# Kernel optimization log

Hardware: AMD Instinct MI355X
Metric: run time of the kernel (lower is better)

Reference implementation:

```python
import jax, jax.numpy as jnp
import numpy as np

EMB = 1024
FF = 4096
NE = 8
TOPK = 2
TEMP = 1.0


def setup_inputs() -> dict:
    key = jax.random.key(0)
    ks = jax.random.split(key, 8)
    s_emb = 1.0 / np.sqrt(EMB)
    s_ff = 1.0 / np.sqrt(FF)
    x = jax.random.normal(ks[0], (4, 2048, EMB), dtype=jnp.float32)
    gate_W = jax.random.uniform(ks[1], (EMB, NE), minval=-s_emb, maxval=s_emb, dtype=jnp.float32)
    gate_b = jax.random.uniform(ks[2], (NE,), minval=-s_emb, maxval=s_emb, dtype=jnp.float32)
    W1 = jax.random.uniform(ks[3], (NE, EMB, FF), minval=-s_emb, maxval=s_emb, dtype=jnp.float32)
    b1 = jax.random.uniform(ks[4], (NE, FF), minval=-s_emb, maxval=s_emb, dtype=jnp.float32)
    W2 = jax.random.uniform(ks[5], (NE, FF, EMB), minval=-s_ff, maxval=s_ff, dtype=jnp.float32)
    b2 = jax.random.uniform(ks[6], (NE, EMB), minval=-s_ff, maxval=s_ff, dtype=jnp.float32)
    return {"x": x, "gate_W": gate_W, "gate_b": gate_b, "W1": W1, "b1": b1, "W2": W2, "b2": b2}


def reference(x, gate_W, gate_b, W1, b1, W2, b2):
    B, S, D = x.shape
    xf = x.reshape(-1, D)  # [T, D]
    T = xf.shape[0]

    gate_logits = (xf @ gate_W + gate_b) / TEMP            # [T, E]
    gate_scores = jax.nn.softmax(gate_logits, axis=-1)     # [T, E]
    topk_scores, topk_idx = jax.lax.top_k(gate_scores, TOPK)
    topk_scores = topk_scores / jnp.sum(topk_scores, axis=-1, keepdims=True)

    # combine_weights[t, e] = sum_i topk_scores[t, i] * (topk_idx[t, i] == e)
    onehot = jax.nn.one_hot(topk_idx, NE, dtype=xf.dtype)  # [T, K, E]
    combine = jnp.einsum('tk,tke->te', topk_scores, onehot)  # [T, E]

    # Dense per-expert FFN (dropout is identity in eval): h = gelu(x W1 + b1); y = h W2 + b2
    h = jax.nn.gelu(jnp.einsum('td,edf->etf', xf, W1) + b1[:, None, :], approximate=False)
    y = jnp.einsum('etf,efd->etd', h, W2) + b2[:, None, :]  # [E, T, D]
    out = jnp.einsum('te,etd->td', combine, y).reshape(B, S, D)

    # Load-balance auxiliary loss
    expert_counts = jnp.sum(onehot, axis=(0, 1))            # [E]
    expert_fraction = expert_counts / (T * TOPK)
    routing_weights = jnp.mean(gate_scores, axis=0)
    aux_loss = NE * jnp.sum(expert_fraction * routing_weights)
    return out, aux_loss
```

## Files before the change

### kernel.cpp

```cpp
#include <hip/hip_runtime.h>
#include <math.h>

#define EMB 1024
#define FF  4096
#define NE  8
#define TTOK 8192

typedef __attribute__((ext_vector_type(4))) float  f32x4;
typedef __attribute__((ext_vector_type(8))) __bf16 bf16x8;
typedef __attribute__((ext_vector_type(4))) __bf16 bf16x4;

#define MAXROWS  18432

#define WS_COUNTS  0
#define WS_CURSORS 1024
#define WS_SSUM    1056
#define WS_NTILES  2080
#define WS_BASE    2084
#define WS_TILE_E  2176
#define WS_TILE_RB 2816
#define WS_TKIDX   4096
#define WS_TKW     69632
#define WS_SLOT    135168
#define WS_TOKID   200704
#define WS_ROWW    274432
#define WS_BIG2    350208

#define SZ_W1T ((size_t)NE * EMB * FF * 2)
#define SZ_W2T ((size_t)NE * EMB * FF * 2)
#define SZ_XB  ((size_t)TTOK * EMB * 2)
#define SZ_H   ((size_t)MAXROWS * FF * 2)
#define SZ_Y   ((size_t)MAXROWS * EMB * 4)

__device__ inline f32x4 fzero() { f32x4 v = {0.f, 0.f, 0.f, 0.f}; return v; }

__device__ __forceinline__ void gl16(const void* g, void* l) {
    __builtin_amdgcn_global_load_lds(
        (const __attribute__((address_space(1))) void*)g,
        (__attribute__((address_space(3))) void*)l, 16, 0, 0);
}

#define DSR(dst, addr, off) \
    asm volatile("ds_read_b128 %0, %1 offset:" #off : "=v"(dst) : "v"(addr))

__device__ __forceinline__ float gelu_f(float v) {
    float u = fabsf(v) * 0.70710678118654752f;
    float p = 1.0f + u * (0.278393f + u * (0.230389f + u * (0.000972f + u * 0.078108f)));
    p = p * p; p = p * p;
    float er = 1.0f - 1.0f / p;
    float s = (v >= 0.0f) ? er : -er;
    return 0.5f * v * (1.0f + s);
}

__global__ __launch_bounds__(256) void gate_kernel(
    const float* __restrict__ x, const float* __restrict__ gW, const float* __restrict__ gb,
    int* counts, float* ssum, int* tk_idx, float* tk_w, __bf16* __restrict__ xb)
{
    int wave = threadIdx.x >> 6;
    int lane = threadIdx.x & 63;
    int t = blockIdx.x * 4 + wave;

    float acc[NE];
#pragma unroll
    for (int e = 0; e < NE; e++) acc[e] = 0.f;

    const float* xr = x + (size_t)t * EMB;
    __bf16* xbr = xb + (size_t)t * EMB;
#pragma unroll
    for (int i = 0; i < 4; i++) {
        int d0 = i * 256 + lane * 4;
        f32x4 xv = *(const f32x4*)(xr + d0);
        bf16x4 cv;
#pragma unroll
        for (int q = 0; q < 4; q++) cv[q] = (__bf16)xv[q];
        *(bf16x4*)(xbr + d0) = cv;
#pragma unroll
        for (int j = 0; j < 4; j++) {
            const float* wrow = gW + (size_t)(d0 + j) * NE;
            float xs = xv[j];
#pragma unroll
            for (int e = 0; e < NE; e++) acc[e] += xs * wrow[e];
        }
    }
#pragma unroll
    for (int e = 0; e < NE; e++) {
#pragma unroll
        for (int off = 32; off; off >>= 1) acc[e] += __shfl_xor(acc[e], off, 64);
    }
    if (lane == 0) {
        float sc[NE];
        float m = -1e30f;
        for (int e = 0; e < NE; e++) { sc[e] = acc[e] + gb[e]; m = fmaxf(m, sc[e]); }
        float sum = 0.f;
        for (int e = 0; e < NE; e++) { sc[e] = expf(sc[e] - m); sum += sc[e]; }
        float inv = 1.f / sum;
        for (int e = 0; e < NE; e++) sc[e] *= inv;
        int i0 = 0; float s0 = sc[0];
        for (int e = 1; e < NE; e++) if (sc[e] > s0) { s0 = sc[e]; i0 = e; }
        int i1 = -1; float s1 = -1e30f;
        for (int e = 0; e < NE; e++) if (e != i0 && sc[e] > s1) { s1 = sc[e]; i1 = e; }
        float rn = 1.f / (s0 + s1);
        tk_idx[2 * t]     = i0;  tk_idx[2 * t + 1] = i1;
        tk_w[2 * t]       = s0 * rn;  tk_w[2 * t + 1] = s1 * rn;
        int slot = blockIdx.x & 31;
        atomicAdd(&counts[i0 * 32 + slot], 1);
        atomicAdd(&counts[i1 * 32 + slot], 1);
        for (int e = 0; e < NE; e++) atomicAdd(&ssum[e * 32 + slot], sc[e]);
    }
}

__global__ void route_build_kernel(const int* counts, const float* ssum,
                                   int* ntiles, int* base, int* tile_e, int* tile_rb,
                                   float* out_aux)
{
    if (threadIdx.x != 0 || blockIdx.x != 0) return;
    int total = 0, tiles = 0;
    float aux = 0.f;
    for (int e = 0; e < NE; e++) {
        int c = 0; float ss = 0.f;
        for (int j = 0; j < 32; j++) { c += counts[e * 32 + j]; ss += ssum[e * 32 + j]; }
        base[e] = total;
        int nt = (c + 255) >> 8;
        for (int i = 0; i < nt; i++) { tile_e[tiles] = e; tile_rb[tiles] = total + (i << 8); tiles++; }
        total += nt << 8;
        aux += ((float)c / (float)(TTOK * 2)) * (ss / (float)TTOK);
    }
    *ntiles = tiles;
    *out_aux = aux * (float)NE;
}

__global__ __launch_bounds__(256) void scatter_kernel(
    const int* __restrict__ tk_idx, const float* __restrict__ tk_w,
    const int* __restrict__ base, int* cursors, int* token_id, float* roww,
    int* slot_of)
{
    int t = blockIdx.x * 256 + threadIdx.x;
#pragma unroll
    for (int k = 0; k < 2; k++) {
        int e = tk_idx[2 * t + k];
        int pos = atomicAdd(&cursors[e], 1);
        int slot = base[e] + pos;
        token_id[slot] = t;
        roww[slot] = tk_w[2 * t + k];
        slot_of[2 * t + k] = slot;
    }
}

__global__ __launch_bounds__(256) void combine_kernel(
    const float* __restrict__ y0, const float* __restrict__ y1, int nsplit,
    const int* __restrict__ slot_of,
    const int* __restrict__ tk_idx, const float* __restrict__ tk_w,
    const float* __restrict__ b2, float* __restrict__ out)
{
    int t = blockIdx.x;
    int dq = threadIdx.x * 4;
    int s0 = slot_of[2 * t], s1 = slot_of[2 * t + 1];
    int e0 = tk_idx[2 * t], e1 = tk_idx[2 * t + 1];
    float w0 = tk_w[2 * t], w1 = tk_w[2 * t + 1];
    f32x4 ya = *(const f32x4*)(y0 + (size_t)s0 * EMB + dq);
    f32x4 yb = *(const f32x4*)(y0 + (size_t)s1 * EMB + dq);
    if (nsplit == 2) {
        f32x4 za = *(const f32x4*)(y1 + (size_t)s0 * EMB + dq);
        f32x4 zb = *(const f32x4*)(y1 + (size_t)s1 * EMB + dq);
#pragma unroll
        for (int q = 0; q < 4; q++) { ya[q] += za[q]; yb[q] += zb[q]; }
    }
    f32x4 ba = *(const f32x4*)(b2 + (size_t)e0 * EMB + dq);
    f32x4 bb = *(const f32x4*)(b2 + (size_t)e1 * EMB + dq);
    f32x4 r;
#pragma unroll
    for (int q = 0; q < 4; q++) r[q] = w0 * (ya[q] + ba[q]) + w1 * (yb[q] + bb[q]);
    *(f32x4*)(out + (size_t)t * EMB + dq) = r;
}

__global__ __launch_bounds__(256) void transpose_cvt2_kernel(
    const float* __restrict__ W1, __bf16* __restrict__ W1T,
    const float* __restrict__ W2, __bf16* __restrict__ W2T)
{
    int f = blockIdx.x;
    int which = f >> 13; f &= 8191;
    int e = f >> 10; f &= 1023;
    int R, C, bx, by;
    const float* src; __bf16* dst;
    if (which == 0) { R = EMB; C = FF;  bx = f & 15; by = f >> 4; src = W1; dst = W1T; }
    else            { R = FF;  C = EMB; bx = f & 63; by = f >> 6; src = W2; dst = W2T; }
    src += (size_t)e * R * C;
    dst += (size_t)e * R * C;
    __shared__ __bf16 Ls[64 * 72];
    int t = threadIdx.x;
    int r0 = bx * 64, c0 = by * 64;
    int ri = t >> 4, cj = (t & 15) * 4;
#pragma unroll
    for (int p = 0; p < 4; p++) {
        int r = ri + p * 16;
        f32x4 v = *(const f32x4*)(src + (size_t)(r0 + r) * C + c0 + cj);
#pragma unroll
        for (int q = 0; q < 4; q++) Ls[(cj + q) * 72 + r] = (__bf16)v[q];
    }
    __syncthreads();
    int c = t >> 2, rq = (t & 3) * 16;
    bf16x8 a = *(bf16x8*)&Ls[c * 72 + rq];
    bf16x8 b = *(bf16x8*)&Ls[c * 72 + rq + 8];
    *(bf16x8*)(dst + (size_t)(c0 + c) * R + r0 + rq) = a;
    *(bf16x8*)(dst + (size_t)(c0 + c) * R + r0 + rq + 8) = b;
}


__global__ __launch_bounds__(512, 2) void gemm1_8p(
    const __bf16* __restrict__ xb, const __bf16* __restrict__ W1T,
    const float* __restrict__ b1,
    const int* __restrict__ token_id, const int* __restrict__ tile_e,
    const int* __restrict__ tile_rb, const int* __restrict__ ntiles,
    __bf16* __restrict__ h)
{
    extern __shared__ __bf16 lds[];
    int flat = blockIdx.x;
    int c8 = flat & 7, r = flat >> 3;
    int mti = r >> 4, nb = r & 15;
    int mt = c8 * 9 + mti;
    if (mt >= *ntiles) return;
    int e = tile_e[mt], rb = tile_rb[mt];
    int n0 = nb * 256;

    int tid = threadIdx.x, lane = tid & 63, wid = tid >> 6;
    int wr = wid >> 2, wc = wid & 3;
    int cl = lane & 15, cq = lane >> 4;

    int srow = tid >> 2;
    int schunk = (tid & 3) ^ ((tid >> 3) & 3);
    const __bf16* ag[2];
#pragma unroll
    for (int hm = 0; hm < 2; hm++) {
        int tok = token_id[rb + hm * 128 + srow];
        if (tok < 0) tok = 0;
        ag[hm] = xb + (size_t)tok * EMB + schunk * 8;
    }
    const __bf16* bg[2];
#pragma unroll
    for (int hn = 0; hn < 2; hn++)
        bg[hn] = W1T + ((size_t)e * FF + (size_t)(n0 + hn * 128 + srow)) * EMB + schunk * 8;

    int sdA0 = wid * 512, sdA1 = 4096 + wid * 512;
    int sdB0 = 8192 + wid * 512, sdB1 = 12288 + wid * 512;

    uint32_t lb = (uint32_t)(uintptr_t)(__attribute__((address_space(3))) __bf16*)lds;
    int xoffe = (cq ^ ((cl >> 1) & 3)) * 8;
    uint32_t ab0 = lb + 2u * (uint32_t)(wr * 4096 + cl * 32 + xoffe);
    uint32_t bb0 = lb + 2u * (uint32_t)(8192 + (wc >> 1) * 4096 + ((wc & 1) * 64 + cl) * 32 + xoffe);

    f32x4 acc[8][4];
#pragma unroll
    for (int i = 0; i < 8; i++)
#pragma unroll
        for (int j = 0; j < 4; j++) acc[i][j] = fzero();

    const int NT = EMB / 32;
#pragma unroll
    for (int t0 = 0; t0 < 3; t0++) {
        __bf16* bp = lds + t0 * 16384;
        int k0 = t0 * 32;
        gl16(ag[0] + k0, bp + sdA0);
        gl16(ag[1] + k0, bp + sdA1);
        gl16(bg[0] + k0, bp + sdB0);
        gl16(bg[1] + k0, bp + sdB1);
    }
    asm volatile("s_waitcnt vmcnt(8)" ::: "memory");
    __builtin_amdgcn_s_barrier();

#pragma unroll 1
    for (int t = 0; t < NT; t++) {
        uint32_t cboff = (uint32_t)(t & 3) * 32768u;
        uint32_t aaddr = ab0 + cboff, baddr = bb0 + cboff;
        bf16x8 b[4], a[8];
        DSR(b[0], baddr, 0);    DSR(b[1], baddr, 1024);
        DSR(b[2], baddr, 2048); DSR(b[3], baddr, 3072);
        DSR(a[0], aaddr, 0);    DSR(a[1], aaddr, 1024);
        DSR(a[2], aaddr, 2048); DSR(a[3], aaddr, 3072);
        DSR(a[4], aaddr, 4096); DSR(a[5], aaddr, 5120);
        DSR(a[6], aaddr, 6144); DSR(a[7], aaddr, 7168);

        int kt = t + 3;
        if (kt < NT) {
            __bf16* sp = lds + (kt & 3) * 16384;
            int ko = kt * 32;
            gl16(ag[0] + ko, sp + sdA0);
            gl16(ag[1] + ko, sp + sdA1);
            gl16(bg[0] + ko, sp + sdB0);
            gl16(bg[1] + ko, sp + sdB1);
        }

        asm volatile("s_waitcnt lgkmcnt(0)" ::: "memory");
        __builtin_amdgcn_sched_barrier(0);
        __builtin_amdgcn_s_setprio(1);
#pragma unroll
        for (int mi = 0; mi < 8; mi++)
#pragma unroll
            for (int ni = 0; ni < 4; ni++)
                acc[mi][ni] = __builtin_amdgcn_mfma_f32_16x16x32_bf16(a[mi], b[ni], acc[mi][ni], 0, 0, 0);
        __builtin_amdgcn_s_setprio(0);

        if (t < NT - 3)       { asm volatile("s_waitcnt vmcnt(8)" ::: "memory"); }
        else if (t == NT - 3) { asm volatile("s_waitcnt vmcnt(4)" ::: "memory"); }
        else if (t == NT - 2) { asm volatile("s_waitcnt vmcnt(0)" ::: "memory"); }
        if (t < NT - 1) __builtin_amdgcn_s_barrier();
    }

    const float* b1g = b1 + (size_t)e * FF + n0;
#pragma unroll
    for (int mi = 0; mi < 8; mi++) {
#pragma unroll
        for (int ni = 0; ni < 4; ni++) {
            int col = wc * 64 + ni * 16 + cl;
            float bias = b1g[col];
#pragma unroll
            for (int j = 0; j < 4; j++) {
                int row = wr * 128 + mi * 16 + cq * 4 + j;
                float v = acc[mi][ni][j] + bias;
                h[(size_t)(rb + row) * FF + n0 + col] = (__bf16)gelu_f(v);
            }
        }
    }
}

__global__ __launch_bounds__(512, 2) void gemm2_8p(
    const __bf16* __restrict__ h, const __bf16* __restrict__ W2T,
    const int* __restrict__ tile_e, const int* __restrict__ tile_rb,
    const int* __restrict__ ntiles,
    float* __restrict__ y0, float* __restrict__ y1, int nsplit)
{
    extern __shared__ __bf16 lds[];
    int flat = blockIdx.x;
    int c8 = flat & 7, r = flat >> 3;
    int z = r / 36; int r36 = r - z * 36;
    int mti = r36 >> 2, nb = r36 & 3;
    int mt = c8 * 9 + mti;
    if (mt >= *ntiles) return;
    int e = tile_e[mt], rb = tile_rb[mt];
    int n0 = nb * 256;
    int KC = FF / nsplit;
    int koff = z * KC;
    float* y = z ? y1 : y0;

    int tid = threadIdx.x, lane = tid & 63, wid = tid >> 6;
    int wr = wid >> 2, wc = wid & 3;
    int cl = lane & 15, cq = lane >> 4;

    int srow = tid >> 2;
    int schunk = (tid & 3) ^ ((tid >> 3) & 3);
    const __bf16* ag[2];
#pragma unroll
    for (int hm = 0; hm < 2; hm++)
        ag[hm] = h + (size_t)(rb + hm * 128 + srow) * FF + koff + schunk * 8;
    const __bf16* bg[2];
#pragma unroll
    for (int hn = 0; hn < 2; hn++)
        bg[hn] = W2T + ((size_t)e * EMB + (size_t)(n0 + hn * 128 + srow)) * FF + koff + schunk * 8;

    int sdA0 = wid * 512, sdA1 = 4096 + wid * 512;
    int sdB0 = 8192 + wid * 512, sdB1 = 12288 + wid * 512;

    uint32_t lb = (uint32_t)(uintptr_t)(__attribute__((address_space(3))) __bf16*)lds;
    int xoffe = (cq ^ ((cl >> 1) & 3)) * 8;
    uint32_t ab0 = lb + 2u * (uint32_t)(wr * 4096 + cl * 32 + xoffe);
    uint32_t bb0 = lb + 2u * (uint32_t)(8192 + (wc >> 1) * 4096 + ((wc & 1) * 64 + cl) * 32 + xoffe);

    f32x4 acc[8][4];
#pragma unroll
    for (int i = 0; i < 8; i++)
#pragma unroll
        for (int j = 0; j < 4; j++) acc[i][j] = fzero();

    const int NT = KC / 32;
#pragma unroll
    for (int t0 = 0; t0 < 3; t0++) {
        __bf16* bp = lds + t0 * 16384;
        int k0 = t0 * 32;
        gl16(ag[0] + k0, bp + sdA0);
        gl16(ag[1] + k0, bp + sdA1);
        gl16(bg[0] + k0, bp + sdB0);
        gl16(bg[1] + k0, bp + sdB1);
    }
    asm volatile("s_waitcnt vmcnt(8)" ::: "memory");
    __builtin_amdgcn_s_barrier();

#pragma unroll 1
    for (int t = 0; t < NT; t++) {
        uint32_t cboff = (uint32_t)(t & 3) * 32768u;
        uint32_t aaddr = ab0 + cboff, baddr = bb0 + cboff;
        bf16x8 b[4], a[8];
        DSR(b[0], baddr, 0);    DSR(b[1], baddr, 1024);
        DSR(b[2], baddr, 2048); DSR(b[3], baddr, 3072);
        DSR(a[0], aaddr, 0);    DSR(a[1], aaddr, 1024);
        DSR(a[2], aaddr, 2048); DSR(a[3], aaddr, 3072);
        DSR(a[4], aaddr, 4096); DSR(a[5], aaddr, 5120);
        DSR(a[6], aaddr, 6144); DSR(a[7], aaddr, 7168);

        int kt = t + 3;
        if (kt < NT) {
            __bf16* sp = lds + (kt & 3) * 16384;
            int ko = kt * 32;
            gl16(ag[0] + ko, sp + sdA0);
            gl16(ag[1] + ko, sp + sdA1);
            gl16(bg[0] + ko, sp + sdB0);
            gl16(bg[1] + ko, sp + sdB1);
        }

        asm volatile("s_waitcnt lgkmcnt(0)" ::: "memory");
        __builtin_amdgcn_sched_barrier(0);
        __builtin_amdgcn_s_setprio(1);
#pragma unroll
        for (int mi = 0; mi < 8; mi++)
#pragma unroll
            for (int ni = 0; ni < 4; ni++)
                acc[mi][ni] = __builtin_amdgcn_mfma_f32_16x16x32_bf16(a[mi], b[ni], acc[mi][ni], 0, 0, 0);
        __builtin_amdgcn_s_setprio(0);

        if (t < NT - 3)       { asm volatile("s_waitcnt vmcnt(8)" ::: "memory"); }
        else if (t == NT - 3) { asm volatile("s_waitcnt vmcnt(4)" ::: "memory"); }
        else if (t == NT - 2) { asm volatile("s_waitcnt vmcnt(0)" ::: "memory"); }
        if (t < NT - 1) __builtin_amdgcn_s_barrier();
    }

#pragma unroll
    for (int mi = 0; mi < 8; mi++) {
#pragma unroll
        for (int ni = 0; ni < 4; ni++) {
            int col = wc * 64 + ni * 16 + cl;
#pragma unroll
            for (int j = 0; j < 4; j++) {
                int row = wr * 128 + mi * 16 + cq * 4 + j;
                y[(size_t)(rb + row) * EMB + n0 + col] = acc[mi][ni][j];
            }
        }
    }
}

extern "C" void kernel_launch(void* const* d_in, const int* in_sizes, int n_in,
                              void* d_out, int out_size, void* d_ws, size_t ws_size,
                              hipStream_t stream)
{
    const float* x   = (const float*)d_in[0];
    const float* gW  = (const float*)d_in[1];
    const float* gb  = (const float*)d_in[2];
    const float* W1  = (const float*)d_in[3];
    const float* b1  = (const float*)d_in[4];
    const float* W2  = (const float*)d_in[5];
    const float* b2  = (const float*)d_in[6];
    float* out = (float*)d_out;

    char* ws = (char*)d_ws;
    int*   counts  = (int*)(ws + WS_COUNTS);
    int*   cursors = (int*)(ws + WS_CURSORS);
    float* ssum    = (float*)(ws + WS_SSUM);
    int*   ntiles  = (int*)(ws + WS_NTILES);
    int*   base    = (int*)(ws + WS_BASE);
    int*   tile_e  = (int*)(ws + WS_TILE_E);
    int*   tile_rb = (int*)(ws + WS_TILE_RB);
    int*   tk_idx  = (int*)(ws + WS_TKIDX);
    float* tk_w    = (float*)(ws + WS_TKW);
    int*   slot_of = (int*)(ws + WS_SLOT);
    int*   token_id= (int*)(ws + WS_TOKID);
    float* roww    = (float*)(ws + WS_ROWW);

    __bf16* W1T  = (__bf16*)(ws + WS_BIG2);
    __bf16* xb   = (__bf16*)(ws + WS_BIG2 + SZ_W1T);
    __bf16* W2T  = (__bf16*)(ws + WS_BIG2 + SZ_W1T + SZ_XB);
    __bf16* hbuf = (__bf16*)(ws + WS_BIG2 + SZ_W1T + SZ_XB + SZ_W2T);
    size_t fixedend = WS_BIG2 + SZ_W1T + SZ_XB + SZ_W2T;

    float* y0 = (float*)(ws + WS_BIG2);
    float* y1 = (float*)(ws + fixedend + SZ_H);
    int nsplit = (ws_size >= fixedend + SZ_H + SZ_Y) ? 2 : 1;

    hipFuncSetAttribute((const void*)gemm1_8p, hipFuncAttributeMaxDynamicSharedMemorySize, 131072);
    hipFuncSetAttribute((const void*)gemm2_8p, hipFuncAttributeMaxDynamicSharedMemorySize, 131072);

    hipMemsetAsync(ws + WS_COUNTS, 0, 2080, stream);
    hipMemsetAsync(ws + WS_TOKID, 0xFF, (size_t)MAXROWS * 4, stream);

    transpose_cvt2_kernel<<<16384, 256, 0, stream>>>(W1, W1T, W2, W2T);

    gate_kernel<<<TTOK / 4, 256, 0, stream>>>(x, gW, gb, counts, ssum, tk_idx, tk_w, xb);
    route_build_kernel<<<1, 64, 0, stream>>>(counts, ssum, ntiles, base, tile_e, tile_rb,
                                             out + (size_t)TTOK * EMB);
    scatter_kernel<<<TTOK / 256, 256, 0, stream>>>(tk_idx, tk_w, base, cursors, token_id, roww, slot_of);

    gemm1_8p<<<8 * 9 * 16, 512, 131072, stream>>>(
        xb, W1T, b1, token_id, tile_e, tile_rb, ntiles, hbuf);
    gemm2_8p<<<8 * 9 * 4 * nsplit, 512, 131072, stream>>>(
        hbuf, W2T, tile_e, tile_rb, ntiles, y0, y1, nsplit);
    combine_kernel<<<TTOK, 256, 0, stream>>>(y0, y1, nsplit, slot_of, tk_idx, tk_w, b2, out);
}
```

Before: 691.4 us.

## Pre-pack routed token rows for gemm1 and store expert outputs in bf16

Adds a pack kernel that gathers routed token rows of x into a contiguous per-slot buffer, so gemm1 reads its A operand with plain strided addressing instead of gathering through token_id. gemm2 partial outputs are now stored in bf16 rather than fp32, which halves the write and combine read traffic and frees workspace for the packed buffer. The cost is an extra kernel launch plus one more pass over the routed activations, and the bf16 rounding of the split-K partial sums before they are combined.

```diff
diff --git a/kernel.cpp b/kernel.cpp
--- a/kernel.cpp
+++ b/kernel.cpp
@@ -30,7 +30,8 @@
 #define SZ_W2T ((size_t)NE * EMB * FF * 2)
 #define SZ_XB  ((size_t)TTOK * EMB * 2)
 #define SZ_H   ((size_t)MAXROWS * FF * 2)
-#define SZ_Y   ((size_t)MAXROWS * EMB * 4)
+#define SZ_XG  ((size_t)MAXROWS * EMB * 2)
+#define SZ_Y2  ((size_t)MAXROWS * EMB * 2)
 
 __device__ inline f32x4 fzero() { f32x4 v = {0.f, 0.f, 0.f, 0.f}; return v; }
 
@@ -146,8 +147,21 @@
     }
 }
 
+__global__ __launch_bounds__(256) void pack_x_kernel(
+    const __bf16* __restrict__ xb, const int* __restrict__ token_id,
+    __bf16* __restrict__ xg)
+{
+    int tid = threadIdx.x;
+    int slot = blockIdx.x * 2 + (tid >> 7);
+    int off = (tid & 127) * 8;
+    int tok = token_id[slot];
+    uint4 v = {0u, 0u, 0u, 0u};
+    if (tok >= 0) v = *(const uint4*)(xb + (size_t)tok * EMB + off);
+    *(uint4*)(xg + (size_t)slot * EMB + off) = v;
+}
+
 __global__ __launch_bounds__(256) void combine_kernel(
-    const float* __restrict__ y0, const float* __restrict__ y1, int nsplit,
+    const __bf16* __restrict__ y0, const __bf16* __restrict__ y1, int nsplit,
     const int* __restrict__ slot_of,
     const int* __restrict__ tk_idx, const float* __restrict__ tk_w,
     const float* __restrict__ b2, float* __restrict__ out)
@@ -157,13 +171,16 @@
     int s0 = slot_of[2 * t], s1 = slot_of[2 * t + 1];
     int e0 = tk_idx[2 * t], e1 = tk_idx[2 * t + 1];
     float w0 = tk_w[2 * t], w1 = tk_w[2 * t + 1];
-    f32x4 ya = *(const f32x4*)(y0 + (size_t)s0 * EMB + dq);
-    f32x4 yb = *(const f32x4*)(y0 + (size_t)s1 * EMB + dq);
+    bf16x4 va = *(const bf16x4*)(y0 + (size_t)s0 * EMB + dq);
+    bf16x4 vb = *(const bf16x4*)(y0 + (size_t)s1 * EMB + dq);
+    f32x4 ya, yb;
+#pragma unroll
+    for (int q = 0; q < 4; q++) { ya[q] = (float)va[q]; yb[q] = (float)vb[q]; }
     if (nsplit == 2) {
-        f32x4 za = *(const f32x4*)(y1 + (size_t)s0 * EMB + dq);
-        f32x4 zb = *(const f32x4*)(y1 + (size_t)s1 * EMB + dq);
-#pragma unroll
-        for (int q = 0; q < 4; q++) { ya[q] += za[q]; yb[q] += zb[q]; }
+        bf16x4 za = *(const bf16x4*)(y1 + (size_t)s0 * EMB + dq);
+        bf16x4 zb = *(const bf16x4*)(y1 + (size_t)s1 * EMB + dq);
+#pragma unroll
+        for (int q = 0; q < 4; q++) { ya[q] += (float)za[q]; yb[q] += (float)zb[q]; }
     }
     f32x4 ba = *(const f32x4*)(b2 + (size_t)e0 * EMB + dq);
     f32x4 bb = *(const f32x4*)(b2 + (size_t)e1 * EMB + dq);
@@ -206,8 +223,9 @@
 }
 
 
+template <bool PACKED>
 __global__ __launch_bounds__(512, 2) void gemm1_8p(
-    const __bf16* __restrict__ xb, const __bf16* __restrict__ W1T,
+    const __bf16* __restrict__ xsrc, const __bf16* __restrict__ W1T,
     const float* __restrict__ b1,
     const int* __restrict__ token_id, const int* __restrict__ tile_e,
     const int* __restrict__ tile_rb, const int* __restrict__ ntiles,
@@ -231,9 +249,13 @@
     const __bf16* ag[2];
 #pragma unroll
     for (int hm = 0; hm < 2; hm++) {
-        int tok = token_id[rb + hm * 128 + srow];
-        if (tok < 0) tok = 0;
-        ag[hm] = xb + (size_t)tok * EMB + schunk * 8;
+        if (PACKED) {
+            ag[hm] = xsrc + (size_t)(rb + hm * 128 + srow) * EMB + schunk * 8;
+        } else {
+            int tok = token_id[rb + hm * 128 + srow];
+            if (tok < 0) tok = 0;
+            ag[hm] = xsrc + (size_t)tok * EMB + schunk * 8;
+        }
     }
     const __bf16* bg[2];
 #pragma unroll
@@ -326,7 +348,7 @@
     const __bf16* __restrict__ h, const __bf16* __restrict__ W2T,
     const int* __restrict__ tile_e, const int* __restrict__ tile_rb,
     const int* __restrict__ ntiles,
-    float* __restrict__ y0, float* __restrict__ y1, int nsplit)
+    __bf16* __restrict__ y0, __bf16* __restrict__ y1, int nsplit)
 {
     extern __shared__ __bf16 lds[];
     int flat = blockIdx.x;
@@ -339,7 +361,7 @@
     int n0 = nb * 256;
     int KC = FF / nsplit;
     int koff = z * KC;
-    float* y = z ? y1 : y0;
+    __bf16* y = z ? y1 : y0;
 
     int tid = threadIdx.x, lane = tid & 63, wid = tid >> 6;
     int wr = wid >> 2, wc = wid & 3;
@@ -429,7 +451,7 @@
 #pragma unroll
             for (int j = 0; j < 4; j++) {
                 int row = wr * 128 + mi * 16 + cq * 4 + j;
-                y[(size_t)(rb + row) * EMB + n0 + col] = acc[mi][ni][j];
+                y[(size_t)(rb + row) * EMB + n0 + col] = (__bf16)acc[mi][ni][j];
             }
         }
     }
@@ -468,11 +490,14 @@
     __bf16* hbuf = (__bf16*)(ws + WS_BIG2 + SZ_W1T + SZ_XB + SZ_W2T);
     size_t fixedend = WS_BIG2 + SZ_W1T + SZ_XB + SZ_W2T;
 
-    float* y0 = (float*)(ws + WS_BIG2);
-    float* y1 = (float*)(ws + fixedend + SZ_H);
-    int nsplit = (ws_size >= fixedend + SZ_H + SZ_Y) ? 2 : 1;
-
-    hipFuncSetAttribute((const void*)gemm1_8p, hipFuncAttributeMaxDynamicSharedMemorySize, 131072);
+    __bf16* y0 = (__bf16*)(ws + WS_BIG2);
+    __bf16* xg = (__bf16*)(ws + fixedend + SZ_H);
+    bool packed = (ws_size >= fixedend + SZ_H + SZ_XG);
+    __bf16* y1 = (__bf16*)(ws + fixedend + SZ_H + (packed ? SZ_XG : 0));
+    int nsplit = (ws_size >= fixedend + SZ_H + (packed ? SZ_XG : 0) + SZ_Y2) ? 2 : 1;
+
+    hipFuncSetAttribute((const void*)gemm1_8p<true>,  hipFuncAttributeMaxDynamicSharedMemorySize, 131072);
+    hipFuncSetAttribute((const void*)gemm1_8p<false>, hipFuncAttributeMaxDynamicSharedMemorySize, 131072);
     hipFuncSetAttribute((const void*)gemm2_8p, hipFuncAttributeMaxDynamicSharedMemorySize, 131072);
 
     hipMemsetAsync(ws + WS_COUNTS, 0, 2080, stream);
@@ -485,8 +510,14 @@
                                              out + (size_t)TTOK * EMB);
     scatter_kernel<<<TTOK / 256, 256, 0, stream>>>(tk_idx, tk_w, base, cursors, token_id, roww, slot_of);
 
-    gemm1_8p<<<8 * 9 * 16, 512, 131072, stream>>>(
-        xb, W1T, b1, token_id, tile_e, tile_rb, ntiles, hbuf);
+    if (packed) {
+        pack_x_kernel<<<MAXROWS / 2, 256, 0, stream>>>(xb, token_id, xg);
+        gemm1_8p<true><<<8 * 9 * 16, 512, 131072, stream>>>(
+            xg, W1T, b1, token_id, tile_e, tile_rb, ntiles, hbuf);
+    } else {
+        gemm1_8p<false><<<8 * 9 * 16, 512, 131072, stream>>>(
+            xb, W1T, b1, token_id, tile_e, tile_rb, ntiles, hbuf);
+    }
     gemm2_8p<<<8 * 9 * 4 * nsplit, 512, 131072, stream>>>(
         hbuf, W2T, tile_e, tile_rb, ntiles, y0, y1, nsplit);
     combine_kernel<<<TTOK, 256, 0, stream>>>(y0, y1, nsplit, slot_of, tk_idx, tk_w, b2, out);
```

Result: no change. 685.5 us (-0.9%).
